# Optimization experiments

Measured on AMD Instinct MI355X. Metric: run time of the kernel, lower is better.

## Reference

```python
import jax, jax.numpy as jnp
import numpy as np
from jax import lax

TAGSET = 32
START = 30  # tag_to_ix[START_TAG]
STOP = 31   # tag_to_ix[STOP_TAG]
# tag 0 is PAD

def setup_inputs() -> dict:
    key = jax.random.key(0)
    k1, k2, k3, k4 = jax.random.split(key, 4)
    B, L, T = 1024, 512, TAGSET
    feats = jax.random.normal(k1, (B, L, T), jnp.float32)
    transitions = jax.random.normal(k2, (T, T), jnp.float32) * 0.1
    word_seq_lens = jax.random.randint(k4, (B,), 1, L + 1)  # in [1, L]
    raw_tags = jax.random.randint(k3, (B, L), 1, 30)  # real tags in [1,30)
    pos = jnp.arange(L)[None, :]
    tags = jnp.where(pos < word_seq_lens[:, None], raw_tags, 0)  # PAD=0 beyond length
    return {"feats": feats, "transitions": transitions, "tags": tags,
            "word_seq_lens": word_seq_lens}


def _crf_nll(feats, transitions, tags, word_seq_lens):
    B, L, T = feats.shape

    # ---- forward algorithm (partition function), forward_pred ----
    # all_scores[b,l,i,j] = transitions[i,j] + feats[b,l,j]  (never materialized)
    alpha0 = transitions[START][None, :] + feats[:, 0]  # (B,T)

    def step(alpha, feat_t):
        # alpha:(B,T) over 'from' tag i; score[b,i,j] = alpha[b,i]+trans[i,j]+feat_t[b,j]
        m = alpha[:, :, None] + transitions[None, :, :] + feat_t[:, None, :]
        new = jax.nn.logsumexp(m, axis=1)  # (B,T)
        return new, new

    feats_t = jnp.swapaxes(feats, 0, 1)  # (L,B,T)
    _, alphas_rest = lax.scan(step, alpha0, feats_t[1:])
    alphas = jnp.concatenate([alpha0[None], alphas_rest], axis=0)  # (L,B,T)

    last_alpha = alphas[word_seq_lens - 1, jnp.arange(B)]  # (B,T) at position len-1
    last_alpha = last_alpha + transitions[:, STOP][None, :]
    forward_score = jnp.sum(jax.nn.logsumexp(last_alpha, axis=1))

    # ---- gold score, forward_labeled ----
    # currentTagScores[b,l,i] = transitions[i, tags[b,l]] + feats[b,l,tags[b,l]]
    emit = jnp.take_along_axis(feats, tags[:, :, None], axis=2)[:, :, 0]  # (B,L)
    cur = transitions.T[tags] + emit[:, :, None]  # (B,L,T)

    begin = cur[:, 0, START]  # (B,)
    end_tag = jnp.take_along_axis(tags, word_seq_lens[:, None] - 1, axis=1)[:, 0]
    end = transitions[end_tag, STOP]  # (B,)
    middle = jnp.take_along_axis(cur[:, 1:, :], tags[:, :L - 1, None], axis=2)[:, :, 0]
    mask = (tags[:, 1:] != 0).astype(feats.dtype)
    gold_score = jnp.sum(begin) + jnp.sum(end) + jnp.sum(middle * mask)

    return forward_score - gold_score


def reference(feats, transitions, tags, word_seq_lens):
    return _crf_nll(feats, transitions, tags, word_seq_lens)
```

## Files before the change

### kernel.cpp

```cpp
#include <hip/hip_runtime.h>

#define NTAG 32
#define START 30
#define STOP 31
#define LOG2E 1.44269504088896340736f
#define LN2 0.69314718055994530942f

typedef float f2 __attribute__((ext_vector_type(2)));
typedef float f4 __attribute__((ext_vector_type(4)));

__device__ __forceinline__ float fexp2(float x) {
#if __has_builtin(__builtin_amdgcn_exp2f)
    return __builtin_amdgcn_exp2f(x);
#else
    return exp2f(x);
#endif
}
__device__ __forceinline__ float flog2(float x) {
#if __has_builtin(__builtin_amdgcn_logf)
    return __builtin_amdgcn_logf(x);
#else
    return log2f(x);
#endif
}

__device__ __forceinline__ void plswap(float &a, float &b) {
#if __has_builtin(__builtin_amdgcn_permlane32_swap)
    auto r = __builtin_amdgcn_permlane32_swap(__float_as_int(a), __float_as_int(b),
                                              false, false);
    a = __int_as_float(r[0]);
    b = __int_as_float(r[1]);
#else
    asm volatile("v_permlane32_swap_b32 %0, %1" : "+v"(a), "+v"(b));
#endif
}

#define PKMUL(d, s, e) asm("v_pk_mul_f32 %0, %1, %2" : "=v"(d) : "v"(s), "v"(e))
#define PKFMA(d, s, e) asm("v_pk_fma_f32 %0, %1, %2, %0" : "+v"(d) : "v"(s), "v"(e))
#define PKADD(d, x, y) asm("v_pk_add_f32 %0, %1, %2" : "=v"(d) : "v"(x), "v"(y))

#define REPEAT8(M) M(0) M(1) M(2) M(3) M(4) M(5) M(6) M(7)

#define STEP_CORE(fraw_, PRE, RN) { \
    const float F_ = fexp2((fraw_) * LOG2E); \
    const float y_ = (PRE) ? (S * F_) : S; \
    *swr = y_; \
    asm volatile("" ::: "memory"); \
    const f4 Q0 = srd4[0], Q1 = srd4[1], Q2 = srd4[2], Q3 = srd4[3]; \
    const f2 s0 = __builtin_shufflevector(Q0, Q0, 0, 1), s1 = __builtin_shufflevector(Q0, Q0, 2, 3); \
    const f2 s2 = __builtin_shufflevector(Q1, Q1, 0, 1), s3 = __builtin_shufflevector(Q1, Q1, 2, 3); \
    const f2 s4 = __builtin_shufflevector(Q2, Q2, 0, 1), s5 = __builtin_shufflevector(Q2, Q2, 2, 3); \
    const f2 s6 = __builtin_shufflevector(Q3, Q3, 0, 1), s7 = __builtin_shufflevector(Q3, Q3, 2, 3); \
    f2 a0, a1, a2, a3; \
    PKMUL(a0, s0, E2_0); PKMUL(a1, s1, E2_1); PKMUL(a2, s2, E2_2); PKMUL(a3, s3, E2_3); \
    PKFMA(a0, s4, E2_4); PKFMA(a1, s5, E2_5); PKFMA(a2, s6, E2_6); PKFMA(a3, s7, E2_7); \
    f2 t01, t23, tt; \
    PKADD(t01, a0, a1); PKADD(t23, a2, a3); PKADD(tt, t01, t23); \
    const float part_ = tt.x + tt.y; \
    float px_ = part_, py_ = part_; \
    plswap(px_, py_); \
    const float r_ = px_ + py_; \
    S = (PRE) ? r_ : (r_ * F_); \
    if (RN) { \
        const int b0_ = __builtin_amdgcn_readfirstlane(__float_as_int(S)); \
        const int k_ = ((b0_ >> 23) & 0xff) - 127; \
        S = __int_as_float(__float_as_int(S) - (k_ << 23)); \
        M2i += k_; } }

#define STEP_RELOAD_F(FS, tload, RN) { const float fraw_ = FS; \
    { const int tc_ = ((tload) < L - 1) ? (tload) : (L - 1); \
      FS = frow[tc_ * NTAG + j]; } \
    STEP_CORE(fraw_, 0, RN) }
#define STEP_RELOAD_B(FS, tload, RN) { const float fraw_ = FS; \
    { const int tc_ = ((tload) > 0) ? (tload) : 0; \
      FS = frow[tc_ * NTAG + j]; } \
    STEP_CORE(fraw_, 1, RN) }

#define STEP_NR_F(FS, RN) { const float fraw_ = FS; STEP_CORE(fraw_, 0, RN) }
#define STEP_NR_B(FS, RN) { const float fraw_ = FS; STEP_CORE(fraw_, 1, RN) }

#define PIN_E2 \
    asm volatile("" : "+v"(E2_0), "+v"(E2_1), "+v"(E2_2), "+v"(E2_3), \
                      "+v"(E2_4), "+v"(E2_5), "+v"(E2_6), "+v"(E2_7));

__global__ __launch_bounds__(768, 1) void crf_nll_kernel(
    const float* __restrict__ feats,
    const float* __restrict__ trans,
    const int*   __restrict__ tags,
    const int*   __restrict__ wsl,
    float* __restrict__ out, int B, int L)
{
    __shared__ float strans[NTAG * NTAG];
    __shared__ __align__(16) float sBC[8][104];
    __shared__ float sRes[8][NTAG];
    __shared__ int   sM2[8];
    for (int i = threadIdx.x; i < NTAG * NTAG; i += 768) strans[i] = trans[i];
    __syncthreads();

    const int wave = threadIdx.x >> 6;
    const int lane = threadIdx.x & 63;

    if (wave < 8) {
        const int dir = wave >> 2;
        int b = blockIdx.x * 4 + (wave & 3);
        if (b >= B) b = B - 1;
        b = __builtin_amdgcn_readfirstlane(b);
        const int j = lane & 31;
        const bool up = lane >= 32;
        const int ib = up ? 16 : 0;
        const int n = __builtin_amdgcn_readfirstlane(wsl[b]);
        const int h = (n + 1) >> 1;
        const float* __restrict__ frow = feats + (size_t)b * L * NTAG;

        float* const swr = &sBC[wave][(up ? 68 : 0) + j];
        const f4* const srd4 = (const f4*)&sBC[wave][up ? 16 : 0];
        float S;
        int M2i = 0;

        if (dir == 0) {
#define DECL_E2(k) f2 E2_##k = { fexp2(strans[(ib + 2*(k)) * NTAG + j] * LOG2E), \
                                 fexp2(strans[(ib + 2*(k) + 1) * NTAG + j] * LOG2E) };
            REPEAT8(DECL_E2)
#undef DECL_E2
            S = fexp2((strans[START * NTAG + j] + frow[j]) * LOG2E);
#define LDF(t_) frow[(((t_) < L - 1) ? (t_) : (L - 1)) * NTAG + j]
            float fA0 = LDF(1),  fA1 = LDF(2),  fA2 = LDF(3),  fA3 = LDF(4),
                  fA4 = LDF(5),  fA5 = LDF(6),  fA6 = LDF(7),  fA7 = LDF(8);
            float fB0 = LDF(9),  fB1 = LDF(10), fB2 = LDF(11), fB3 = LDF(12),
                  fB4 = LDF(13), fB5 = LDF(14), fB6 = LDF(15), fB7 = LDF(16);
#undef LDF
            int t = 1;
            for (; t + 16 <= h; t += 16) {
                PIN_E2
                STEP_RELOAD_F(fA0, t + 16, 0)
                STEP_RELOAD_F(fA1, t + 17, 0)
                STEP_RELOAD_F(fA2, t + 18, 0)
                STEP_RELOAD_F(fA3, t + 19, 1)
                STEP_RELOAD_F(fA4, t + 20, 0)
                STEP_RELOAD_F(fA5, t + 21, 0)
                STEP_RELOAD_F(fA6, t + 22, 0)
                STEP_RELOAD_F(fA7, t + 23, 1)
                STEP_RELOAD_F(fB0, t + 24, 0)
                STEP_RELOAD_F(fB1, t + 25, 0)
                STEP_RELOAD_F(fB2, t + 26, 0)
                STEP_RELOAD_F(fB3, t + 27, 1)
                STEP_RELOAD_F(fB4, t + 28, 0)
                STEP_RELOAD_F(fB5, t + 29, 0)
                STEP_RELOAD_F(fB6, t + 30, 0)
                STEP_RELOAD_F(fB7, t + 31, 1)
            }
            if (t + 0  < h) { STEP_NR_F(fA0, 1) }
            if (t + 1  < h) { STEP_NR_F(fA1, 1) }
            if (t + 2  < h) { STEP_NR_F(fA2, 1) }
            if (t + 3  < h) { STEP_NR_F(fA3, 1) }
            if (t + 4  < h) { STEP_NR_F(fA4, 1) }
            if (t + 5  < h) { STEP_NR_F(fA5, 1) }
            if (t + 6  < h) { STEP_NR_F(fA6, 1) }
            if (t + 7  < h) { STEP_NR_F(fA7, 1) }
            if (t + 8  < h) { STEP_NR_F(fB0, 1) }
            if (t + 9  < h) { STEP_NR_F(fB1, 1) }
            if (t + 10 < h) { STEP_NR_F(fB2, 1) }
            if (t + 11 < h) { STEP_NR_F(fB3, 1) }
            if (t + 12 < h) { STEP_NR_F(fB4, 1) }
            if (t + 13 < h) { STEP_NR_F(fB5, 1) }
            if (t + 14 < h) { STEP_NR_F(fB6, 1) }
        } else {
#define DECL_E2(k) f2 E2_##k = { fexp2(strans[j * NTAG + ib + 2*(k)] * LOG2E), \
                                 fexp2(strans[j * NTAG + ib + 2*(k) + 1] * LOG2E) };
            REPEAT8(DECL_E2)
#undef DECL_E2
            S = fexp2(strans[j * NTAG + STOP] * LOG2E);
            const int cnt = n - h;
#define LDB(s_) frow[(((n - 1 - (s_)) > 0) ? (n - 1 - (s_)) : 0) * NTAG + j]
            float gA0 = LDB(0),  gA1 = LDB(1),  gA2 = LDB(2),  gA3 = LDB(3),
                  gA4 = LDB(4),  gA5 = LDB(5),  gA6 = LDB(6),  gA7 = LDB(7);
            float gB0 = LDB(8),  gB1 = LDB(9),  gB2 = LDB(10), gB3 = LDB(11),
                  gB4 = LDB(12), gB5 = LDB(13), gB6 = LDB(14), gB7 = LDB(15);
#undef LDB
            int s = 0;
            for (; s + 16 <= cnt; s += 16) {
                PIN_E2
                STEP_RELOAD_B(gA0, n - 1 - (s + 0)  - 16, 0)
                STEP_RELOAD_B(gA1, n - 1 - (s + 1)  - 16, 0)
                STEP_RELOAD_B(gA2, n - 1 - (s + 2)  - 16, 0)
                STEP_RELOAD_B(gA3, n - 1 - (s + 3)  - 16, 1)
                STEP_RELOAD_B(gA4, n - 1 - (s + 4)  - 16, 0)
                STEP_RELOAD_B(gA5, n - 1 - (s + 5)  - 16, 0)
                STEP_RELOAD_B(gA6, n - 1 - (s + 6)  - 16, 0)
                STEP_RELOAD_B(gA7, n - 1 - (s + 7)  - 16, 1)
                STEP_RELOAD_B(gB0, n - 1 - (s + 8)  - 16, 0)
                STEP_RELOAD_B(gB1, n - 1 - (s + 9)  - 16, 0)
                STEP_RELOAD_B(gB2, n - 1 - (s + 10) - 16, 0)
                STEP_RELOAD_B(gB3, n - 1 - (s + 11) - 16, 1)
                STEP_RELOAD_B(gB4, n - 1 - (s + 12) - 16, 0)
                STEP_RELOAD_B(gB5, n - 1 - (s + 13) - 16, 0)
                STEP_RELOAD_B(gB6, n - 1 - (s + 14) - 16, 0)
                STEP_RELOAD_B(gB7, n - 1 - (s + 15) - 16, 1)
            }
            if (s + 0  < cnt) { STEP_NR_B(gA0, 1) }
            if (s + 1  < cnt) { STEP_NR_B(gA1, 1) }
            if (s + 2  < cnt) { STEP_NR_B(gA2, 1) }
            if (s + 3  < cnt) { STEP_NR_B(gA3, 1) }
            if (s + 4  < cnt) { STEP_NR_B(gA4, 1) }
            if (s + 5  < cnt) { STEP_NR_B(gA5, 1) }
            if (s + 6  < cnt) { STEP_NR_B(gA6, 1) }
            if (s + 7  < cnt) { STEP_NR_B(gA7, 1) }
            if (s + 8  < cnt) { STEP_NR_B(gB0, 1) }
            if (s + 9  < cnt) { STEP_NR_B(gB1, 1) }
            if (s + 10 < cnt) { STEP_NR_B(gB2, 1) }
            if (s + 11 < cnt) { STEP_NR_B(gB3, 1) }
            if (s + 12 < cnt) { STEP_NR_B(gB4, 1) }
            if (s + 13 < cnt) { STEP_NR_B(gB5, 1) }
            if (s + 14 < cnt) { STEP_NR_B(gB6, 1) }
        }
        if (!up) {
            sRes[wave][j] = S;
            if (j == 0) sM2[wave] = M2i;
        }
    } else {
        int b = blockIdx.x * 4 + (wave - 8);
        if (b < B) {
            b = __builtin_amdgcn_readfirstlane(b);
            const int n = wsl[b];
            const float* __restrict__ frow = feats + (size_t)b * L * NTAG;
            const int*   __restrict__ trow = tags  + (size_t)b * L;
            float acc = 0.f;
            for (int tt = lane; tt < L; tt += 64) {
                const int tg = trow[tt];
                if (tt == 0) {
                    acc += strans[START * NTAG + tg] + frow[tg];
                } else if (tt < n) {
                    const int tgp = trow[tt - 1];
                    acc += strans[tgp * NTAG + tg] + frow[tt * NTAG + tg];
                }
                if (tt == n - 1) {
                    acc += strans[tg * NTAG + STOP];
                }
            }
#pragma unroll
            for (int k = 1; k < 64; k <<= 1) acc += __shfl_xor(acc, k, 64);
            if (lane == 0) atomicAdd(out, -acc);
        }
    }

    __syncthreads();

    if (wave < 4) {
        const int b2 = blockIdx.x * 4 + wave;
        if (b2 < B && lane < 32) {
            float ex = sRes[wave][lane] * sRes[wave + 4][lane];
#pragma unroll
            for (int k = 1; k < 32; k <<= 1) ex += __shfl_xor(ex, k, 32);
            if (lane == 0)
                atomicAdd(out, LN2 * ((float)(sM2[wave] + sM2[wave + 4]) + flog2(ex)));
        }
    }
}

extern "C" void kernel_launch(void* const* d_in, const int* in_sizes, int n_in,
                              void* d_out, int out_size, void* d_ws, size_t ws_size,
                              hipStream_t stream) {
    const float* feats = (const float*)d_in[0];
    const float* trans = (const float*)d_in[1];
    const int*   tags  = (const int*)d_in[2];
    const int*   wsl   = (const int*)d_in[3];
    float* out = (float*)d_out;

    const int B = in_sizes[3];
    const int L = in_sizes[2] / B;

    (void)hipMemsetAsync(out, 0, sizeof(float), stream);
    const int grid = (B + 3) / 4;
    crf_nll_kernel<<<grid, 768, 0, stream>>>(feats, trans, tags, wsl, out, B, L);
}
```

Baseline: 127.6 us.

## Replace LDS broadcast in CRF recurrence with DPP row rotations and permlane swaps

The per-step 32x32 matrix-vector product no longer writes the alpha vector to shared memory and reads it back as vectors. Lanes are now arranged as four 16-lane rows, and the product uses DPP row_ror-modified mul/fmac instructions against 16 pre-rotated exp-transition registers, with permlane32/permlane16 swaps to combine the partial sums. The aim is to take LDS write/read latency off the serial dependency chain. In exchange it adds s_nop hazards and extra cross-lane swaps, and it gives up the packed FMA instructions.

New measurement: 132.7 us. +3.9%, slower.

```diff
diff --git a/kernel.cpp b/kernel.cpp
--- a/kernel.cpp
+++ b/kernel.cpp
@@ -6,9 +6,6 @@
 #define LOG2E 1.44269504088896340736f
 #define LN2 0.69314718055994530942f
 
-typedef float f2 __attribute__((ext_vector_type(2)));
-typedef float f4 __attribute__((ext_vector_type(4)));
-
 __device__ __forceinline__ float fexp2(float x) {
 #if __has_builtin(__builtin_amdgcn_exp2f)
     return __builtin_amdgcn_exp2f(x);
@@ -24,43 +21,57 @@
 #endif
 }
 
-__device__ __forceinline__ void plswap(float &a, float &b) {
+__device__ __forceinline__ void plswap32(float &a, float &b) {
 #if __has_builtin(__builtin_amdgcn_permlane32_swap)
     auto r = __builtin_amdgcn_permlane32_swap(__float_as_int(a), __float_as_int(b),
                                               false, false);
     a = __int_as_float(r[0]);
     b = __int_as_float(r[1]);
 #else
-    asm volatile("v_permlane32_swap_b32 %0, %1" : "+v"(a), "+v"(b));
-#endif
-}
-
-#define PKMUL(d, s, e) asm("v_pk_mul_f32 %0, %1, %2" : "=v"(d) : "v"(s), "v"(e))
-#define PKFMA(d, s, e) asm("v_pk_fma_f32 %0, %1, %2, %0" : "+v"(d) : "v"(s), "v"(e))
-#define PKADD(d, x, y) asm("v_pk_add_f32 %0, %1, %2" : "=v"(d) : "v"(x), "v"(y))
-
-#define REPEAT8(M) M(0) M(1) M(2) M(3) M(4) M(5) M(6) M(7)
+    asm volatile("s_nop 1\n\tv_permlane32_swap_b32 %0, %1" : "+v"(a), "+v"(b));
+#endif
+}
+__device__ __forceinline__ void plswap16(float &a, float &b) {
+#if __has_builtin(__builtin_amdgcn_permlane16_swap)
+    auto r = __builtin_amdgcn_permlane16_swap(__float_as_int(a), __float_as_int(b),
+                                              false, false);
+    a = __int_as_float(r[0]);
+    b = __int_as_float(r[1]);
+#else
+    asm volatile("s_nop 1\n\tv_permlane16_swap_b32 %0, %1" : "+v"(a), "+v"(b));
+#endif
+}
+
+#define DPP_ROR_I(x, R) __builtin_amdgcn_update_dpp(0, (x), 0x120 + (R), 0xf, 0xf, false)
+
+#define REPEAT15(M) \
+    M(1) M(2) M(3) M(4) M(5) M(6) M(7) M(8) \
+    M(9) M(10) M(11) M(12) M(13) M(14) M(15)
+
+#define MROT(r, A) asm volatile("v_mul_f32 %0, %1, %2 row_ror:" #r \
+                                : "=v"(A) : "v"(y_), "v"(E_##r));
+#define FROT(r, A) asm volatile("v_fmac_f32 %0, %1, %2 row_ror:" #r \
+                                : "+v"(A) : "v"(y_), "v"(E_##r));
 
 #define STEP_CORE(fraw_, PRE, RN) { \
     const float F_ = fexp2((fraw_) * LOG2E); \
     const float y_ = (PRE) ? (S * F_) : S; \
-    *swr = y_; \
-    asm volatile("" ::: "memory"); \
-    const f4 Q0 = srd4[0], Q1 = srd4[1], Q2 = srd4[2], Q3 = srd4[3]; \
-    const f2 s0 = __builtin_shufflevector(Q0, Q0, 0, 1), s1 = __builtin_shufflevector(Q0, Q0, 2, 3); \
-    const f2 s2 = __builtin_shufflevector(Q1, Q1, 0, 1), s3 = __builtin_shufflevector(Q1, Q1, 2, 3); \
-    const f2 s4 = __builtin_shufflevector(Q2, Q2, 0, 1), s5 = __builtin_shufflevector(Q2, Q2, 2, 3); \
-    const f2 s6 = __builtin_shufflevector(Q3, Q3, 0, 1), s7 = __builtin_shufflevector(Q3, Q3, 2, 3); \
-    f2 a0, a1, a2, a3; \
-    PKMUL(a0, s0, E2_0); PKMUL(a1, s1, E2_1); PKMUL(a2, s2, E2_2); PKMUL(a3, s3, E2_3); \
-    PKFMA(a0, s4, E2_4); PKFMA(a1, s5, E2_5); PKFMA(a2, s6, E2_6); PKFMA(a3, s7, E2_7); \
-    f2 t01, t23, tt; \
-    PKADD(t01, a0, a1); PKADD(t23, a2, a3); PKADD(tt, t01, t23); \
-    const float part_ = tt.x + tt.y; \
+    float a0, a1, a2, a3; \
+    a0 = y_ * E_0; \
+    asm volatile("s_nop 1");  \
+    MROT(1, a1) MROT(2, a2) MROT(3, a3) \
+    FROT(4, a0) FROT(5, a1) FROT(6, a2) FROT(7, a3) \
+    FROT(8, a0) FROT(9, a1) FROT(10, a2) FROT(11, a3) \
+    FROT(12, a0) FROT(13, a1) FROT(14, a2) FROT(15, a3) \
+    const float part_ = (a0 + a1) + (a2 + a3); \
     float px_ = part_, py_ = part_; \
-    plswap(px_, py_); \
-    const float r_ = px_ + py_; \
-    S = (PRE) ? r_ : (r_ * F_); \
+    plswap32(px_, py_); \
+    const float tot_ = px_ + py_; \
+    const float val_ = (PRE) ? tot_ : (tot_ * F_); \
+    float tx_ = val_, ty_ = val_; \
+    plswap16(tx_, ty_); \
+    const float corr_ = (tx_ + ty_) - val_;    \
+    S = needX ? corr_ : val_; \
     if (RN) { \
         const int b0_ = __builtin_amdgcn_readfirstlane(__float_as_int(S)); \
         const int k_ = ((b0_ >> 23) & 0xff) - 127; \
@@ -69,19 +80,21 @@
 
 #define STEP_RELOAD_F(FS, tload, RN) { const float fraw_ = FS; \
     { const int tc_ = ((tload) < L - 1) ? (tload) : (L - 1); \
-      FS = frow[tc_ * NTAG + j]; } \
+      FS = frow[tc_ * NTAG + fj]; } \
     STEP_CORE(fraw_, 0, RN) }
 #define STEP_RELOAD_B(FS, tload, RN) { const float fraw_ = FS; \
     { const int tc_ = ((tload) > 0) ? (tload) : 0; \
-      FS = frow[tc_ * NTAG + j]; } \
+      FS = frow[tc_ * NTAG + fj]; } \
     STEP_CORE(fraw_, 1, RN) }
 
 #define STEP_NR_F(FS, RN) { const float fraw_ = FS; STEP_CORE(fraw_, 0, RN) }
 #define STEP_NR_B(FS, RN) { const float fraw_ = FS; STEP_CORE(fraw_, 1, RN) }
 
-#define PIN_E2 \
-    asm volatile("" : "+v"(E2_0), "+v"(E2_1), "+v"(E2_2), "+v"(E2_3), \
-                      "+v"(E2_4), "+v"(E2_5), "+v"(E2_6), "+v"(E2_7));
+#define PIN_E \
+    asm volatile("" : "+v"(E_0),  "+v"(E_1),  "+v"(E_2),  "+v"(E_3), \
+                      "+v"(E_4),  "+v"(E_5),  "+v"(E_6),  "+v"(E_7)); \
+    asm volatile("" : "+v"(E_8),  "+v"(E_9),  "+v"(E_10), "+v"(E_11), \
+                      "+v"(E_12), "+v"(E_13), "+v"(E_14), "+v"(E_15));
 
 __global__ __launch_bounds__(768, 1) void crf_nll_kernel(
     const float* __restrict__ feats,
@@ -91,7 +104,6 @@
     float* __restrict__ out, int B, int L)
 {
     __shared__ float strans[NTAG * NTAG];
-    __shared__ __align__(16) float sBC[8][104];
     __shared__ float sRes[8][NTAG];
     __shared__ int   sM2[8];
     for (int i = threadIdx.x; i < NTAG * NTAG; i += 768) strans[i] = trans[i];
@@ -105,25 +117,29 @@
         int b = blockIdx.x * 4 + (wave & 3);
         if (b >= B) b = B - 1;
         b = __builtin_amdgcn_readfirstlane(b);
-        const int j = lane & 31;
-        const bool up = lane >= 32;
-        const int ib = up ? 16 : 0;
+
+        const int row  = lane >> 4;
+        const int j16  = lane & 15;
+        const int hrow = (row == 1 || row == 2) ? 1 : 0;
+        const int htag = j16 + (hrow << 4);
+        const int otag = j16 + ((row & 1) << 4);
+        const bool needX = (row >= 2);
+
         const int n = __builtin_amdgcn_readfirstlane(wsl[b]);
         const int h = (n + 1) >> 1;
         const float* __restrict__ frow = feats + (size_t)b * L * NTAG;
-
-        float* const swr = &sBC[wave][(up ? 68 : 0) + j];
-        const f4* const srd4 = (const f4*)&sBC[wave][up ? 16 : 0];
         float S;
         int M2i = 0;
 
         if (dir == 0) {
-#define DECL_E2(k) f2 E2_##k = { fexp2(strans[(ib + 2*(k)) * NTAG + j] * LOG2E), \
-                                 fexp2(strans[(ib + 2*(k) + 1) * NTAG + j] * LOG2E) };
-            REPEAT8(DECL_E2)
-#undef DECL_E2
-            S = fexp2((strans[START * NTAG + j] + frow[j]) * LOG2E);
-#define LDF(t_) frow[(((t_) < L - 1) ? (t_) : (L - 1)) * NTAG + j]
+            float E_0 = fexp2(strans[htag * NTAG + otag] * LOG2E);
+#define DECL_E(r) const int q##r = DPP_ROR_I(htag, r); \
+                  float E_##r = fexp2(strans[q##r * NTAG + otag] * LOG2E);
+            REPEAT15(DECL_E)
+#undef DECL_E
+            const int fj = otag;
+            S = fexp2((strans[START * NTAG + htag] + frow[htag]) * LOG2E);
+#define LDF(t_) frow[(((t_) < L - 1) ? (t_) : (L - 1)) * NTAG + fj]
             float fA0 = LDF(1),  fA1 = LDF(2),  fA2 = LDF(3),  fA3 = LDF(4),
                   fA4 = LDF(5),  fA5 = LDF(6),  fA6 = LDF(7),  fA7 = LDF(8);
             float fB0 = LDF(9),  fB1 = LDF(10), fB2 = LDF(11), fB3 = LDF(12),
@@ -131,7 +147,7 @@
 #undef LDF
             int t = 1;
             for (; t + 16 <= h; t += 16) {
-                PIN_E2
+                PIN_E
                 STEP_RELOAD_F(fA0, t + 16, 0)
                 STEP_RELOAD_F(fA1, t + 17, 0)
                 STEP_RELOAD_F(fA2, t + 18, 0)
@@ -165,13 +181,15 @@
             if (t + 13 < h) { STEP_NR_F(fB5, 1) }
             if (t + 14 < h) { STEP_NR_F(fB6, 1) }
         } else {
-#define DECL_E2(k) f2 E2_##k = { fexp2(strans[j * NTAG + ib + 2*(k)] * LOG2E), \
-                                 fexp2(strans[j * NTAG + ib + 2*(k) + 1] * LOG2E) };
-            REPEAT8(DECL_E2)
-#undef DECL_E2
-            S = fexp2(strans[j * NTAG + STOP] * LOG2E);
+            float E_0 = fexp2(strans[otag * NTAG + htag] * LOG2E);
+#define DECL_E(r) const int q##r = DPP_ROR_I(htag, r); \
+                  float E_##r = fexp2(strans[otag * NTAG + q##r] * LOG2E);
+            REPEAT15(DECL_E)
+#undef DECL_E
+            const int fj = htag;
+            S = fexp2(strans[htag * NTAG + STOP] * LOG2E);
             const int cnt = n - h;
-#define LDB(s_) frow[(((n - 1 - (s_)) > 0) ? (n - 1 - (s_)) : 0) * NTAG + j]
+#define LDB(s_) frow[(((n - 1 - (s_)) > 0) ? (n - 1 - (s_)) : 0) * NTAG + fj]
             float gA0 = LDB(0),  gA1 = LDB(1),  gA2 = LDB(2),  gA3 = LDB(3),
                   gA4 = LDB(4),  gA5 = LDB(5),  gA6 = LDB(6),  gA7 = LDB(7);
             float gB0 = LDB(8),  gB1 = LDB(9),  gB2 = LDB(10), gB3 = LDB(11),
@@ -179,7 +197,7 @@
 #undef LDB
             int s = 0;
             for (; s + 16 <= cnt; s += 16) {
-                PIN_E2
+                PIN_E
                 STEP_RELOAD_B(gA0, n - 1 - (s + 0)  - 16, 0)
                 STEP_RELOAD_B(gA1, n - 1 - (s + 1)  - 16, 0)
                 STEP_RELOAD_B(gA2, n - 1 - (s + 2)  - 16, 0)
@@ -213,9 +231,9 @@
             if (s + 13 < cnt) { STEP_NR_B(gB5, 1) }
             if (s + 14 < cnt) { STEP_NR_B(gB6, 1) }
         }
-        if (!up) {
-            sRes[wave][j] = S;
-            if (j == 0) sM2[wave] = M2i;
+        if (lane < 32) {
+            sRes[wave][lane] = S;
+            if (lane == 0) sM2[wave] = M2i;
         }
     } else {
         int b = blockIdx.x * 4 + (wave - 8);
```
